# Kernel optimization log

Measured on AMD Instinct MI355X. Metric: run time of the kernel, lower is better.

Reference implementation:

```python
import jax, jax.numpy as jnp
import numpy as np

B, L, E, H = 4, 2048, 1024, 16
HD = E // H  # head_dim = 64


def setup_inputs() -> dict:
    key = jax.random.key(0)
    ks = jax.random.split(key, 10)
    s = 1.0 / np.sqrt(E)
    return {
        "x": jax.random.normal(ks[0], (B, L, E), dtype=jnp.float32),
        "mask": jax.random.randint(ks[1], (B, L), 0, 2, dtype=jnp.int32),
        "Wq": jax.random.normal(ks[2], (E, E), dtype=jnp.float32) * s,
        "bq": jnp.zeros((E,), dtype=jnp.float32),
        "Wk": jax.random.normal(ks[3], (E, E), dtype=jnp.float32) * s,
        "bk": jnp.zeros((E,), dtype=jnp.float32),
        "Wv": jax.random.normal(ks[4], (E, E), dtype=jnp.float32) * s,
        "bv": jnp.zeros((E,), dtype=jnp.float32),
        "Wo": jax.random.normal(ks[5], (E, E), dtype=jnp.float32) * s,
        "bo": jnp.zeros((E,), dtype=jnp.float32),
    }


def _separate_heads(t):
    # Faithful to the torch code: a raw reshape (B, L, E) -> (B, H, L, HD),
    # NOT the usual (B, L, H, HD) + transpose.
    return t.reshape(B, H, L, HD)


def reference(x, mask, Wq, bq, Wk, bk, Wv, bv, Wo, bo):
    q = _separate_heads(x @ Wq.T + bq)
    k = _separate_heads(x @ Wk.T + bk)
    v = _separate_heads(x @ Wv.T + bv)
    scores = jnp.einsum('bhqd,bhkd->bhqk', q, k) / np.sqrt(HD).astype(np.float32)
    m = mask[:, None, None, :]  # (B,1,1,L) broadcast over (B,H,L,L)
    scores = jnp.where(m == 0, jnp.float32(-1e10), scores)
    attn = jax.nn.softmax(scores, axis=-1)
    out = jnp.einsum('bhqk,bhkd->bhqd', attn, v)
    out = out.transpose(0, 2, 1, 3).reshape(B, L, E)
    return out @ Wo.T + bo
```

## Files before the change

kernel.cpp:

```cpp
#include <hip/hip_runtime.h>
#include <hip/hip_bf16.h>

namespace {
constexpr int kB = 4, kL = 2048, kE = 1024, kH = 16, kHD = 64;
constexpr float kCs = 0.18033688f;
}

typedef __attribute__((ext_vector_type(8))) short bf16x8;
typedef __attribute__((ext_vector_type(4))) float f32x4;

__device__ __forceinline__ short f2bf(float f) {
  __hip_bfloat16 h = __float2bfloat16(f);
  return *reinterpret_cast<short*>(&h);
}

__device__ __forceinline__ void load_lds16(const void* g, void* l) {
  __builtin_amdgcn_global_load_lds((const __attribute__((address_space(1))) void*)g,
                                   (__attribute__((address_space(3))) void*)l, 16, 0, 0);
}
__device__ __forceinline__ void load_lds4(const void* g, void* l) {
  __builtin_amdgcn_global_load_lds((const __attribute__((address_space(1))) void*)g,
                                   (__attribute__((address_space(3))) void*)l, 4, 0, 0);
}

__global__ __launch_bounds__(256) void k_cvt(const float* __restrict__ s,
                                             short* __restrict__ d, int n) {
  int i = (blockIdx.x * 256 + threadIdx.x) * 4;
  if (i < n) {
    float4 v = *reinterpret_cast<const float4*>(s + i);
    short4 o;
    o.x = f2bf(v.x); o.y = f2bf(v.y); o.z = f2bf(v.z); o.w = f2bf(v.w);
    *reinterpret_cast<short4*>(d + i) = o;
  }
}

__global__ __launch_bounds__(256) void k_cvtw(const float* __restrict__ w0,
                                              const float* __restrict__ w1,
                                              const float* __restrict__ w2,
                                              const float* __restrict__ w3,
                                              const int* __restrict__ mask,
                                              short* __restrict__ dst,
                                              float* __restrict__ mkf) {
  int bx = blockIdx.x;
  if (bx >= 4096) {
    int i = (bx - 4096) * 256 + threadIdx.x;
    mkf[i] = mask[i] != 0 ? -10.0f : -1.0e10f;
    return;
  }
  int seg = bx >> 10;
  const float* s = seg == 0 ? w0 : seg == 1 ? w1 : seg == 2 ? w2 : w3;
  int local = ((bx & 1023) * 256 + threadIdx.x) * 4;
  float4 v = *reinterpret_cast<const float4*>(s + local);
  short4 o;
  o.x = f2bf(v.x); o.y = f2bf(v.y); o.z = f2bf(v.z); o.w = f2bf(v.w);
  *reinterpret_cast<short4*>(dst + seg * 1048576 + local) = o;
}

__global__ __launch_bounds__(256) void k_trv(const short* __restrict__ Vl,
                                             short* __restrict__ Vt) {
  __shared__ unsigned T[64 * 33];
  const int t = threadIdx.x;
  const int hb = blockIdx.y;
  const int l0 = blockIdx.x * 64;
  const short* src = Vl + hb * 131072;
  short* dst = Vt + hb * 131072;
  const int d8 = (t & 7) * 8;
  const int lp = t >> 3;
  const uint4 va = *reinterpret_cast<const uint4*>(src + (l0 + 2 * lp) * 64 + d8);
  const uint4 vb = *reinterpret_cast<const uint4*>(src + (l0 + 2 * lp + 1) * 64 + d8);
  const unsigned a[4] = {va.x, va.y, va.z, va.w};
  const unsigned b[4] = {vb.x, vb.y, vb.z, vb.w};
#pragma unroll
  for (int j = 0; j < 4; ++j) {
    unsigned z0 = __builtin_amdgcn_perm(b[j], a[j], 0x05040100u);
    unsigned z1 = __builtin_amdgcn_perm(b[j], a[j], 0x07060302u);
    T[(d8 + 2 * j) * 33 + lp] = z0;
    T[(d8 + 2 * j + 1) * 33 + lp] = z1;
  }
  __syncthreads();
  const int u = (t & 7) * 4;
#pragma unroll
  for (int h2 = 0; h2 < 2; ++h2) {
    int d = (t >> 3) + h2 * 32;
    uint4 r;
    r.x = T[d * 33 + u];     r.y = T[d * 33 + u + 1];
    r.z = T[d * 33 + u + 2]; r.w = T[d * 33 + u + 3];
    *reinterpret_cast<uint4*>(dst + d * 2048 + l0 + u * 2) = r;
  }
}

struct GemmCore256 {
  f32x4 acc[4][4];
  int tid, w, lane, quad, m16, wm, wn;
  __device__ __forceinline__ void run(const short* __restrict__ A,
                                      const short* __restrict__ W,
                                      int bm0, int bn0, short* S) {
    tid = threadIdx.x;
    w = tid >> 6; lane = tid & 63; quad = lane >> 4; m16 = lane & 15;
    wm = (w >> 1) * 64; wn = (w & 1) * 64;
#pragma unroll
    for (int i = 0; i < 4; ++i)
#pragma unroll
      for (int j = 0; j < 4; ++j) acc[i][j] = (f32x4){0, 0, 0, 0};

    const int srow = tid >> 3;
    const int sunit = (tid & 7) ^ (srow & 7);
    const short* Ag = A + (bm0 + srow) * 1024 + sunit * 8;
    const short* Wg = W + (bn0 + srow) * 1024 + sunit * 8;
    const int x7 = m16 & 7;
    const int u0 = (quad ^ x7) * 8;
    const int u1 = u0 ^ 32;
    const int baseA = (wm + m16) * 64;
    const int baseB = 16384 + (wn + m16) * 64;

#define STG_A(Sb, T, c) load_lds16(Ag + (c) * 65536 + (T) * 64, (Sb) + (c) * 4096 + tid * 8)
#define STG_B(Sb, T, c) load_lds16(Wg + (c) * 65536 + (T) * 64, (Sb) + 16384 + (c) * 4096 + tid * 8)

    short* S1 = S + 24576;
    STG_A(S, 0, 0); STG_A(S, 0, 1); STG_A(S, 0, 2); STG_A(S, 0, 3);
    STG_B(S, 0, 0); STG_B(S, 0, 1);
    STG_A(S1, 1, 0); STG_A(S1, 1, 1); STG_A(S1, 1, 2); STG_A(S1, 1, 3);
    STG_B(S1, 1, 0); STG_B(S1, 1, 1);
    asm volatile("s_waitcnt vmcnt(6)" ::: "memory");
    __builtin_amdgcn_s_barrier();
    __builtin_amdgcn_sched_barrier(0);

    int bc = 0;
    for (int t = 0; t < 16; ++t) {
      short* Sc = S + bc * 24576;
      int b2 = bc + 2; if (b2 >= 3) b2 -= 3;
      short* Sp = S + b2 * 24576;
      const bool pf = (t < 14);

      bf16x8 a[4][2], b[4][2];
#pragma unroll
      for (int i = 0; i < 4; ++i) {
        a[i][0] = *reinterpret_cast<const bf16x8*>(&Sc[baseA + i * 1024 + u0]);
        a[i][1] = *reinterpret_cast<const bf16x8*>(&Sc[baseA + i * 1024 + u1]);
      }
#pragma unroll
      for (int j = 0; j < 4; ++j) {
        b[j][0] = *reinterpret_cast<const bf16x8*>(&Sc[baseB + j * 1024 + u0]);
        b[j][1] = *reinterpret_cast<const bf16x8*>(&Sc[baseB + j * 1024 + u1]);
      }
      if (pf) {
        STG_A(Sp, t + 2, 0); STG_A(Sp, t + 2, 1); STG_A(Sp, t + 2, 2); STG_A(Sp, t + 2, 3);
        STG_B(Sp, t + 2, 0); STG_B(Sp, t + 2, 1);
      }
      __builtin_amdgcn_s_setprio(1);
#pragma unroll
      for (int i = 0; i < 4; ++i)
#pragma unroll
        for (int j = 0; j < 4; ++j) {
          acc[i][j] = __builtin_amdgcn_mfma_f32_16x16x32_bf16(a[i][0], b[j][0], acc[i][j], 0, 0, 0);
          acc[i][j] = __builtin_amdgcn_mfma_f32_16x16x32_bf16(a[i][1], b[j][1], acc[i][j], 0, 0, 0);
        }
      __builtin_amdgcn_s_setprio(0);
      if (pf) { asm volatile("s_waitcnt vmcnt(6)" ::: "memory"); }
      else    { asm volatile("s_waitcnt vmcnt(0)" ::: "memory"); }
      __builtin_amdgcn_s_barrier();
      __builtin_amdgcn_sched_barrier(0);
      bc += 1; if (bc >= 3) bc -= 3;
    }
#undef STG_A
#undef STG_B
  }
};

__global__ __launch_bounds__(512, 2) void k_gemm_qkv(const short* __restrict__ xb,
                                                     const short* __restrict__ Wq,
                                                     const short* __restrict__ Wk,
                                                     const short* __restrict__ Wv,
                                                     const float* __restrict__ bq,
                                                     const float* __restrict__ bk,
                                                     const float* __restrict__ bv,
                                                     short* __restrict__ Q,
                                                     short* __restrict__ K,
                                                     short* __restrict__ Vl) {
  __shared__ __attribute__((aligned(16))) short S[73728];
  const int l = blockIdx.x + 24 * blockIdx.y;
  const int xcd = l & 7, wv_ = l >> 3;
  const int bm0 = (xcd + 8 * (wv_ & 3)) * 256;
  const int colsel = wv_ >> 2;
  const int sel = colsel >> 3;
  const int bn0 = (colsel & 7) * 128;
  const short* W = sel == 0 ? Wq : sel == 1 ? Wk : Wv;
  const float* bias = sel == 0 ? bq : sel == 1 ? bk : bv;

  GemmCore256 g;
  g.run(xb, W, bm0, bn0, S);

  float bj[4];
#pragma unroll
  for (int j = 0; j < 4; ++j) bj[j] = bias[bn0 + g.wn + j * 16 + g.m16];

  short* C = sel == 0 ? Q : sel == 1 ? K : Vl;
  float sc = sel == 0 ? kCs : 1.0f;
#pragma unroll
  for (int i = 0; i < 4; ++i)
#pragma unroll
    for (int j = 0; j < 4; ++j)
#pragma unroll
      for (int rg = 0; rg < 4; ++rg) {
        int row = bm0 + g.wm + i * 16 + g.quad * 4 + rg;
        int col = bn0 + g.wn + j * 16 + g.m16;
        C[row * 1024 + col] = f2bf((g.acc[i][j][rg] + bj[j]) * sc);
      }
}

__global__ __launch_bounds__(512, 2) void k_gemm_out(const short* __restrict__ A,
                                                     const short* __restrict__ Wo,
                                                     const float* __restrict__ bo,
                                                     float* __restrict__ C) {
  __shared__ __attribute__((aligned(16))) short S[73728];
  const int l = blockIdx.x + 8 * blockIdx.y;
  const int xcd = l & 7, wv_ = l >> 3;
  const int bm0 = (xcd + 8 * (wv_ & 3)) * 256;
  const int bn0 = (wv_ >> 2) * 128;
  GemmCore256 g;
  g.run(A, Wo, bm0, bn0, S);
  float bj[4];
#pragma unroll
  for (int j = 0; j < 4; ++j) bj[j] = bo[bn0 + g.wn + j * 16 + g.m16];
#pragma unroll
  for (int i = 0; i < 4; ++i)
#pragma unroll
    for (int j = 0; j < 4; ++j)
#pragma unroll
      for (int rg = 0; rg < 4; ++rg) {
        int row = bm0 + g.wm + i * 16 + g.quad * 4 + rg;
        int col = bn0 + g.wn + j * 16 + g.m16;
        C[row * 1024 + col] = g.acc[i][j][rg] + bj[j];
      }
}

__global__ __launch_bounds__(256, 3) void k_attn(const short* __restrict__ Q,
                                                 const short* __restrict__ Km,
                                                 const short* __restrict__ Vt,
                                                 const float* __restrict__ Mg,
                                                 short* __restrict__ Out) {
  __shared__ __attribute__((aligned(16))) short U[8448];
  __shared__ __attribute__((aligned(16))) short Ks[4096];
  __shared__ __attribute__((aligned(16))) short Vs[4096];
  __shared__ __attribute__((aligned(16))) float Mk[64];

  const int tid = threadIdx.x;
  const int w = tid >> 6, lane = tid & 63;
  const int quad = lane >> 4, m16 = lane & 15;
  const int lid = blockIdx.x + 16 * blockIdx.y;
  const int xcd = lid & 7, wv_ = lid >> 3;
  const int hb = xcd + 8 * (wv_ & 7);
  const int qb = wv_ >> 3;
  const int b = hb >> 4, h = hb & 15;
  const int wb = w * 2112;

  const short* Qh = Q + hb * (kL * kHD) + qb * 128 * kHD;
  const short* Kh = Km + hb * (kL * kHD);
  const short* Vh = Vt + hb * (kL * kHD);
  const float* Mb = Mg + b * kL;

  const int srow = tid >> 3;
  const int sunit = (tid & 7) ^ (srow & 7);
  const int x7 = m16 & 7;
  const int u0 = (quad ^ x7) * 8;
  const int u1 = u0 ^ 32;

#pragma unroll
  for (int c = 0; c < 4; ++c)
    load_lds16(Qh + (c * 32 + srow) * 64 + sunit * 8, &U[c * 2048 + tid * 8]);
  __syncthreads();
  bf16x8 qf[2][2];
#pragma unroll
  for (int i = 0; i < 2; ++i) {
    qf[i][0] = *reinterpret_cast<const bf16x8*>(&U[(w * 32 + i * 16 + m16) * 64 + u0]);
    qf[i][1] = *reinterpret_cast<const bf16x8*>(&U[(w * 32 + i * 16 + m16) * 64 + u1]);
  }

  bf16x8 ones;
#pragma unroll
  for (int e = 0; e < 8; ++e) ones[e] = (short)0x3F80;

  f32x4 oacc[2][4] = {};
  f32x4 lacc[2] = {};

  for (int kb = 0; kb < 32; ++kb) {
    int kbase = kb * 64;
    load_lds16(Kh + (kbase + srow) * 64 + sunit * 8, &Ks[tid * 8]);
    load_lds16(Kh + (kbase + 32 + srow) * 64 + sunit * 8, &Ks[2048 + tid * 8]);
    load_lds16(Vh + srow * 2048 + kbase + sunit * 8, &Vs[tid * 8]);
    load_lds16(Vh + (32 + srow) * 2048 + kbase + sunit * 8, &Vs[2048 + tid * 8]);
    load_lds4(Mb + kbase + lane, &Mk[lane]);
    __syncthreads();

    f32x4 ST[4][2];
#pragma unroll
    for (int j = 0; j < 4; ++j) {
      float4 mj4 = *reinterpret_cast<const float4*>(&Mk[j * 16 + quad * 4]);
      f32x4 init; init[0] = mj4.x; init[1] = mj4.y; init[2] = mj4.z; init[3] = mj4.w;
#pragma unroll
      for (int i = 0; i < 2; ++i) ST[j][i] = init;
      bf16x8 kf0 = *reinterpret_cast<const bf16x8*>(&Ks[(j * 16 + m16) * 64 + u0]);
      bf16x8 kf1 = *reinterpret_cast<const bf16x8*>(&Ks[(j * 16 + m16) * 64 + u1]);
#pragma unroll
      for (int i = 0; i < 2; ++i) {
        ST[j][i] = __builtin_amdgcn_mfma_f32_16x16x32_bf16(kf0, qf[i][0], ST[j][i], 0, 0, 0);
        ST[j][i] = __builtin_amdgcn_mfma_f32_16x16x32_bf16(kf1, qf[i][1], ST[j][i], 0, 0, 0);
      }
    }

    const int kc_w = (quad >> 1);
    const int inner = (quad & 1) * 4;
#pragma unroll
    for (int j = 0; j < 4; ++j)
#pragma unroll
      for (int i = 0; i < 2; ++i) {
        float p0 = __builtin_amdgcn_exp2f(ST[j][i][0]);
        float p1 = __builtin_amdgcn_exp2f(ST[j][i][1]);
        float p2 = __builtin_amdgcn_exp2f(ST[j][i][2]);
        float p3 = __builtin_amdgcn_exp2f(ST[j][i][3]);
        uint2 pk;
        pk.x = __builtin_amdgcn_perm(__builtin_bit_cast(unsigned, p1),
                                     __builtin_bit_cast(unsigned, p0), 0x07060302u);
        pk.y = __builtin_amdgcn_perm(__builtin_bit_cast(unsigned, p3),
                                     __builtin_bit_cast(unsigned, p2), 0x07060302u);
        *reinterpret_cast<uint2*>(
            &U[wb + (j * 2 + kc_w) * 264 + (i * 16 + m16) * 8 + inner]) = pk;
      }
    asm volatile("s_waitcnt lgkmcnt(0)" ::: "memory");

    bf16x8 pf[2][2];
#pragma unroll
    for (int i = 0; i < 2; ++i)
#pragma unroll
      for (int s = 0; s < 2; ++s)
        pf[i][s] = *reinterpret_cast<const bf16x8*>(
            &U[wb + (s * 4 + quad) * 264 + (i * 16 + m16) * 8]);

#pragma unroll
    for (int i = 0; i < 2; ++i) {
      lacc[i] = __builtin_amdgcn_mfma_f32_16x16x32_bf16(pf[i][0], ones, lacc[i], 0, 0, 0);
      lacc[i] = __builtin_amdgcn_mfma_f32_16x16x32_bf16(pf[i][1], ones, lacc[i], 0, 0, 0);
    }

#pragma unroll
    for (int j = 0; j < 4; ++j) {
      bf16x8 vf0 = *reinterpret_cast<const bf16x8*>(&Vs[(j * 16 + m16) * 64 + u0]);
      bf16x8 vf1 = *reinterpret_cast<const bf16x8*>(&Vs[(j * 16 + m16) * 64 + u1]);
#pragma unroll
      for (int i = 0; i < 2; ++i) {
        oacc[i][j] = __builtin_amdgcn_mfma_f32_16x16x32_bf16(pf[i][0], vf0, oacc[i][j], 0, 0, 0);
        oacc[i][j] = __builtin_amdgcn_mfma_f32_16x16x32_bf16(pf[i][1], vf1, oacc[i][j], 0, 0, 0);
      }
    }
    __syncthreads();
  }

#pragma unroll
  for (int i = 0; i < 2; ++i)
#pragma unroll
    for (int j = 0; j < 4; ++j) {
      int d = j * 16 + m16;
#pragma unroll
      for (int rg = 0; rg < 4; ++rg) {
        int ql = qb * 128 + w * 32 + i * 16 + quad * 4 + rg;
        Out[(b * kL + ql) * kE + h * kHD + d] =
            f2bf(oacc[i][j][rg] / lacc[i][rg]);
      }
    }
}

extern "C" void kernel_launch(void* const* d_in, const int* in_sizes, int n_in,
                              void* d_out, int out_size, void* d_ws, size_t ws_size,
                              hipStream_t stream) {
  const float* x  = (const float*)d_in[0];
  const int* mask = (const int*)d_in[1];
  const float* Wq = (const float*)d_in[2];
  const float* bq = (const float*)d_in[3];
  const float* Wk = (const float*)d_in[4];
  const float* bk = (const float*)d_in[5];
  const float* Wv = (const float*)d_in[6];
  const float* bv = (const float*)d_in[7];
  const float* Wo = (const float*)d_in[8];
  const float* bo = (const float*)d_in[9];

  short* ws  = (short*)d_ws;
  short* xb  = ws;
  short* Wqb = xb  + 8388608;
  short* Wkb = Wqb + 1048576;
  short* Wvb = Wkb + 1048576;
  short* Wob = Wvb + 1048576;
  short* Qb  = Wob + 1048576;
  short* Kb  = Qb  + 8388608;
  short* Vtb = Kb  + 8388608;
  short* AOb = Vtb + 8388608;
  float* Mkf = (float*)(AOb + 8388608);

  k_cvt<<<8192, 256, 0, stream>>>(x, xb, 8388608);
  k_cvtw<<<4128, 256, 0, stream>>>(Wq, Wk, Wv, Wo, mask, Wqb, Mkf);

  k_gemm_qkv<<<dim3(24, 32), 512, 0, stream>>>(xb, Wqb, Wkb, Wvb, bq, bk, bv, Qb, Kb, AOb);
  k_trv<<<dim3(32, 64), 256, 0, stream>>>(AOb, Vtb);
  k_attn<<<dim3(16, 64), 256, 0, stream>>>(Qb, Kb, Vtb, Mkf, AOb);
  k_gemm_out<<<dim3(8, 32), 512, 0, stream>>>(AOb, Wob, bo, (float*)d_out);
}
```

Baseline: 266.2 us.

## Double-buffer K/V/mask tiles in attention and raise MFMA wave priority

The attention kernel now keeps two LDS buffers for K, V and the mask. It prefetches the next key block while computing on the current one, and uses a single barrier per iteration instead of two __syncthreads. The goal is to hide global-to-LDS load latency behind the MFMA work and cut synchronisation. It also brackets the MFMA sections with s_setprio to favour matrix issue. The cost is roughly twice the K/V LDS, about 50KB per block, which could press on the 3-blocks-per-CU occupancy target.

```diff
diff --git a/kernel.cpp b/kernel.cpp
--- a/kernel.cpp
+++ b/kernel.cpp
@@ -240,9 +240,9 @@
                                                  const float* __restrict__ Mg,
                                                  short* __restrict__ Out) {
   __shared__ __attribute__((aligned(16))) short U[8448];
-  __shared__ __attribute__((aligned(16))) short Ks[4096];
-  __shared__ __attribute__((aligned(16))) short Vs[4096];
-  __shared__ __attribute__((aligned(16))) float Mk[64];
+  __shared__ __attribute__((aligned(16))) short Ks[8192];
+  __shared__ __attribute__((aligned(16))) short Vs[8192];
+  __shared__ __attribute__((aligned(16))) float Mk[128];
 
   const int tid = threadIdx.x;
   const int w = tid >> 6, lane = tid & 63;
@@ -265,6 +265,18 @@
   const int u0 = (quad ^ x7) * 8;
   const int u1 = u0 ^ 32;
 
+#define STAGE_KV(kb_, buf_)                                                        \
+  do {                                                                             \
+    int kbase_ = (kb_) * 64;                                                       \
+    load_lds16(Kh + (kbase_ + srow) * 64 + sunit * 8, &Ks[(buf_) * 4096 + tid * 8]); \
+    load_lds16(Kh + (kbase_ + 32 + srow) * 64 + sunit * 8,                         \
+               &Ks[(buf_) * 4096 + 2048 + tid * 8]);                               \
+    load_lds16(Vh + srow * 2048 + kbase_ + sunit * 8, &Vs[(buf_) * 4096 + tid * 8]); \
+    load_lds16(Vh + (32 + srow) * 2048 + kbase_ + sunit * 8,                       \
+               &Vs[(buf_) * 4096 + 2048 + tid * 8]);                               \
+    load_lds4(Mb + kbase_ + lane, &Mk[(buf_) * 64 + lane]);                        \
+  } while (0)
+
 #pragma unroll
   for (int c = 0; c < 4; ++c)
     load_lds16(Qh + (c * 32 + srow) * 64 + sunit * 8, &U[c * 2048 + tid * 8]);
@@ -283,30 +295,34 @@
   f32x4 oacc[2][4] = {};
   f32x4 lacc[2] = {};
 
+  STAGE_KV(0, 0);
+  asm volatile("s_waitcnt lgkmcnt(0)" ::: "memory");
+
   for (int kb = 0; kb < 32; ++kb) {
-    int kbase = kb * 64;
-    load_lds16(Kh + (kbase + srow) * 64 + sunit * 8, &Ks[tid * 8]);
-    load_lds16(Kh + (kbase + 32 + srow) * 64 + sunit * 8, &Ks[2048 + tid * 8]);
-    load_lds16(Vh + srow * 2048 + kbase + sunit * 8, &Vs[tid * 8]);
-    load_lds16(Vh + (32 + srow) * 2048 + kbase + sunit * 8, &Vs[2048 + tid * 8]);
-    load_lds4(Mb + kbase + lane, &Mk[lane]);
-    __syncthreads();
+    const int cur = kb & 1;
+    const int kvb = cur * 4096;
+    asm volatile("s_waitcnt vmcnt(0)" ::: "memory");
+    __builtin_amdgcn_s_barrier();
+    __builtin_amdgcn_sched_barrier(0);
+    if (kb < 31) STAGE_KV(kb + 1, cur ^ 1);
 
     f32x4 ST[4][2];
+    __builtin_amdgcn_s_setprio(1);
 #pragma unroll
     for (int j = 0; j < 4; ++j) {
-      float4 mj4 = *reinterpret_cast<const float4*>(&Mk[j * 16 + quad * 4]);
+      float4 mj4 = *reinterpret_cast<const float4*>(&Mk[cur * 64 + j * 16 + quad * 4]);
       f32x4 init; init[0] = mj4.x; init[1] = mj4.y; init[2] = mj4.z; init[3] = mj4.w;
 #pragma unroll
       for (int i = 0; i < 2; ++i) ST[j][i] = init;
-      bf16x8 kf0 = *reinterpret_cast<const bf16x8*>(&Ks[(j * 16 + m16) * 64 + u0]);
-      bf16x8 kf1 = *reinterpret_cast<const bf16x8*>(&Ks[(j * 16 + m16) * 64 + u1]);
+      bf16x8 kf0 = *reinterpret_cast<const bf16x8*>(&Ks[kvb + (j * 16 + m16) * 64 + u0]);
+      bf16x8 kf1 = *reinterpret_cast<const bf16x8*>(&Ks[kvb + (j * 16 + m16) * 64 + u1]);
 #pragma unroll
       for (int i = 0; i < 2; ++i) {
         ST[j][i] = __builtin_amdgcn_mfma_f32_16x16x32_bf16(kf0, qf[i][0], ST[j][i], 0, 0, 0);
         ST[j][i] = __builtin_amdgcn_mfma_f32_16x16x32_bf16(kf1, qf[i][1], ST[j][i], 0, 0, 0);
       }
     }
+    __builtin_amdgcn_s_setprio(0);
 
     const int kc_w = (quad >> 1);
     const int inner = (quad & 1) * 4;
@@ -336,6 +352,7 @@
         pf[i][s] = *reinterpret_cast<const bf16x8*>(
             &U[wb + (s * 4 + quad) * 264 + (i * 16 + m16) * 8]);
 
+    __builtin_amdgcn_s_setprio(1);
 #pragma unroll
     for (int i = 0; i < 2; ++i) {
       lacc[i] = __builtin_amdgcn_mfma_f32_16x16x32_bf16(pf[i][0], ones, lacc[i], 0, 0, 0);
@@ -344,16 +361,17 @@
 
 #pragma unroll
     for (int j = 0; j < 4; ++j) {
-      bf16x8 vf0 = *reinterpret_cast<const bf16x8*>(&Vs[(j * 16 + m16) * 64 + u0]);
-      bf16x8 vf1 = *reinterpret_cast<const bf16x8*>(&Vs[(j * 16 + m16) * 64 + u1]);
+      bf16x8 vf0 = *reinterpret_cast<const bf16x8*>(&Vs[kvb + (j * 16 + m16) * 64 + u0]);
+      bf16x8 vf1 = *reinterpret_cast<const bf16x8*>(&Vs[kvb + (j * 16 + m16) * 64 + u1]);
 #pragma unroll
       for (int i = 0; i < 2; ++i) {
         oacc[i][j] = __builtin_amdgcn_mfma_f32_16x16x32_bf16(pf[i][0], vf0, oacc[i][j], 0, 0, 0);
         oacc[i][j] = __builtin_amdgcn_mfma_f32_16x16x32_bf16(pf[i][1], vf1, oacc[i][j], 0, 0, 0);
       }
     }
-    __syncthreads();
-  }
+    __builtin_amdgcn_s_setprio(0);
+  }
+#undef STAGE_KV
 
 #pragma unroll
   for (int i = 0; i < 2; ++i)
```

Measured after the change: 284.3 us. 6.8% more time.
